# Performance work log

Hardware: AMD Instinct MI355X
Metric: run time of the kernel (lower is better)

The kernel has to match this reference:

```python
import jax, jax.numpy as jnp
import numpy as np

D_MODEL = 1024
NUM_HEADS = 16
HEAD_DIM = D_MODEL // NUM_HEADS
THETA = 10000.0


def apply_rope(x, token_positions):
    # x: [B, H, S, d_head]; token_positions: [S] int
    d = x.shape[-1]
    inv_freq = THETA ** (-jnp.arange(0, d, 2, dtype=jnp.float32) / d)  # [d/2]
    ang = token_positions.astype(jnp.float32)[:, None] * inv_freq      # [S, d/2]
    cos, sin = jnp.cos(ang), jnp.sin(ang)
    x1 = x[..., 0::2]
    x2 = x[..., 1::2]
    out_even = x1 * cos - x2 * sin
    out_odd = x1 * sin + x2 * cos
    # interleave even/odd back: [..., S, d/2, 2] -> [..., S, d]
    return jnp.stack([out_even, out_odd], axis=-1).reshape(x.shape)


def setup_inputs() -> dict:
    key = jax.random.key(0)
    ks = jax.random.split(key, 5)
    scale = 1.0 / np.sqrt(D_MODEL)
    x = jax.random.normal(ks[0], (4, 2048, D_MODEL), dtype=jnp.float32)
    wq = jax.random.normal(ks[1], (D_MODEL, D_MODEL), dtype=jnp.float32) * scale
    wk = jax.random.normal(ks[2], (D_MODEL, D_MODEL), dtype=jnp.float32) * scale
    wv = jax.random.normal(ks[3], (D_MODEL, D_MODEL), dtype=jnp.float32) * scale
    wo = jax.random.normal(ks[4], (D_MODEL, D_MODEL), dtype=jnp.float32) * scale
    token_positions = jnp.arange(2048, dtype=jnp.int32)
    return {"x": x, "wq": wq, "wk": wk, "wv": wv, "wo": wo,
            "token_positions": token_positions}


def reference(x, wq, wk, wv, wo, token_positions):
    B, S, D = x.shape
    H, dh = NUM_HEADS, HEAD_DIM
    # fused QKV projection (Linear stores weight [out, in]; y = x @ W.T)
    q = jnp.einsum('bsd,ed->bse', x, wq).reshape(B, S, H, dh).transpose(0, 2, 1, 3)
    k = jnp.einsum('bsd,ed->bse', x, wk).reshape(B, S, H, dh).transpose(0, 2, 1, 3)
    v = jnp.einsum('bsd,ed->bse', x, wv).reshape(B, S, H, dh).transpose(0, 2, 1, 3)
    q = apply_rope(q, token_positions)
    k = apply_rope(k, token_positions)
    scores = jnp.einsum('bhid,bhjd->bhij', q, k) / jnp.sqrt(jnp.float32(dh))
    causal = jnp.tril(jnp.ones((S, S), dtype=bool))
    scores = jnp.where(causal, scores, -jnp.inf)
    attn = jax.nn.softmax(scores, axis=-1)
    out = jnp.einsum('bhij,bhjd->bhid', attn, v)            # [B,H,S,dh]
    out = out.transpose(0, 2, 1, 3).reshape(B, S, D)         # [B,S,D]
    return jnp.einsum('bsd,ed->bse', out, wo)
```

## Files before the change

kernel.cpp:

```cpp
#include <hip/hip_runtime.h>
#include <cstdint>
#include <cstddef>

typedef short bf16x8 __attribute__((ext_vector_type(8)));
typedef float f32x4 __attribute__((ext_vector_type(4)));
typedef unsigned short u16;
typedef u16 u16x4v __attribute__((ext_vector_type(4)));

#define SEQ 2048

static __device__ __forceinline__ u16 f2bf(float f) {
  uint32_t u = __builtin_bit_cast(uint32_t, f);
  u += 0x7fffu + ((u >> 16) & 1u);
  return (u16)(u >> 16);
}
static __device__ __forceinline__ float bf2f(u16 v) {
  uint32_t u = ((uint32_t)v) << 16;
  return __builtin_bit_cast(float, u);
}

#define MFMA_BF16(a, b, c) __builtin_amdgcn_mfma_f32_16x16x32_bf16((a), (b), (c), 0, 0, 0)

static __device__ __forceinline__ void gload_lds16(const void* g, void* l) {
  __builtin_amdgcn_global_load_lds((const __attribute__((address_space(1))) void*)g,
                                   (__attribute__((address_space(3))) void*)l, 16, 0, 0);
}

__global__ __launch_bounds__(256) void cvt_kernel(
    const float4* __restrict__ x, const float4* __restrict__ wq,
    const float4* __restrict__ wk, const float4* __restrict__ wv,
    const float4* __restrict__ wo, u16x4v* __restrict__ xb,
    u16x4v* __restrict__ wqkvb, u16x4v* __restrict__ wob) {
  const int id = blockIdx.x * 256 + threadIdx.x;
  const float4* src;
  u16x4v* dst;
  if (id < 2097152) { src = x + id; dst = xb + id; }
  else if (id < 2359296) { const int j = id - 2097152; src = wq + j; dst = wqkvb + j; }
  else if (id < 2621440) { const int j = id - 2359296; src = wk + j; dst = wqkvb + 262144 + j; }
  else if (id < 2883584) { const int j = id - 2621440; src = wv + j; dst = wqkvb + 524288 + j; }
  else { const int j = id - 2883584; src = wo + j; dst = wob + j; }
  const float4 v = *src;
  u16x4v o;
  o[0] = f2bf(v.x); o[1] = f2bf(v.y); o[2] = f2bf(v.z); o[3] = f2bf(v.w);
  *dst = o;
}

__global__ __launch_bounds__(256) void rope_tbl_kernel(const int* __restrict__ tp,
                                                       float2* __restrict__ tbl) {
  const int id = blockIdx.x * 256 + threadIdx.x;
  const int s = id >> 5, i = id & 31;
  const float pos = (float)tp[s];
  const float freq = powf(10000.0f, -(float)(2 * i) / 64.0f);
  const float ang = pos * freq;
  float sv, cv;
  sincosf(ang, &sv, &cv);
  tbl[id] = make_float2(cv, sv);
}

template <bool OUT_BF16>
__global__ __launch_bounds__(256) void gemm_bt(const u16* __restrict__ A,
                                               const u16* __restrict__ Bt,
                                               void* __restrict__ Cout,
                                               int M, int N, int K) {
  __shared__ __align__(16) u16 As[128 * 64];
  __shared__ __align__(16) u16 Bs[128 * 64];
  const int tid = threadIdx.x;
  const int w = tid >> 6;
  const int l = tid & 63;
  const int g = l >> 4;
  const int lr = l & 15;
  const int wm = (w >> 1) * 64;
  const int wn = (w & 1) * 64;
  const long tile_m = (long)blockIdx.y * 128;
  const long tile_n = (long)blockIdx.x * 128;

  const int lrow = l >> 3;
  const int lcolsw = (l & 7) ^ lrow;

  f32x4 acc[4][4] = {};

  for (int k0 = 0; k0 < K; k0 += 64) {
#pragma unroll
    for (int cc = 0; cc < 4; ++cc) {
      const int c = w * 4 + cc;
      const int row = c * 8 + lrow;
      gload_lds16(A + (tile_m + row) * (long)K + k0 + lcolsw * 8, As + c * 512);
      gload_lds16(Bt + (tile_n + row) * (long)K + k0 + lcolsw * 8, Bs + c * 512);
    }
    __syncthreads();
#pragma unroll
    for (int kk = 0; kk < 2; ++kk) {
      bf16x8 af[4], bfr[4];
#pragma unroll
      for (int mi = 0; mi < 4; ++mi) {
        const int row = wm + mi * 16 + lr;
        const int cc = ((kk << 2) + g) ^ (row & 7);
        af[mi] = *(const bf16x8*)((const char*)As + row * 128 + cc * 16);
      }
#pragma unroll
      for (int ni = 0; ni < 4; ++ni) {
        const int row = wn + ni * 16 + lr;
        const int cc = ((kk << 2) + g) ^ (row & 7);
        bfr[ni] = *(const bf16x8*)((const char*)Bs + row * 128 + cc * 16);
      }
#pragma unroll
      for (int mi = 0; mi < 4; ++mi)
#pragma unroll
        for (int ni = 0; ni < 4; ++ni)
          acc[mi][ni] = MFMA_BF16(af[mi], bfr[ni], acc[mi][ni]);
    }
    __syncthreads();
  }

#pragma unroll
  for (int mi = 0; mi < 4; ++mi) {
#pragma unroll
    for (int ni = 0; ni < 4; ++ni) {
      const long row0 = tile_m + wm + mi * 16 + g * 4;
      const long col = tile_n + wn + ni * 16 + lr;
      if (OUT_BF16) {
        u16* C = (u16*)Cout;
#pragma unroll
        for (int r = 0; r < 4; ++r) C[(row0 + r) * N + col] = f2bf(acc[mi][ni][r]);
      } else {
        float* C = (float*)Cout;
#pragma unroll
        for (int r = 0; r < 4; ++r) C[(row0 + r) * N + col] = acc[mi][ni][r];
      }
    }
  }
}

__global__ __launch_bounds__(256) void rope_kernel(u16* __restrict__ qkvb,
                                                   const float2* __restrict__ tbl) {
  const int id = blockIdx.x * 256 + threadIdx.x;
  const int qk = id >> 22;
  const int r = id & 0x3FFFFF;
  const int row = r >> 9;
  const int p = r & 511;
  const int h = p >> 5, i = p & 31;
  const int s = row & (SEQ - 1);
  const float2 cs = tbl[s * 32 + i];
  uint32_t* ptr = (uint32_t*)(qkvb + (size_t)row * 3072 + qk * 1024 + h * 64 + 2 * i);
  const uint32_t v = *ptr;
  const float x1 = bf2f((u16)(v & 0xffffu));
  const float x2 = bf2f((u16)(v >> 16));
  const float e = x1 * cs.x - x2 * cs.y;
  const float o = x1 * cs.y + x2 * cs.x;
  *ptr = (uint32_t)f2bf(e) | ((uint32_t)f2bf(o) << 16);
}

__global__ __launch_bounds__(256) void transpose_v_kernel(const u16* __restrict__ qkvb,
                                                          u16* __restrict__ Vt) {
  const int bh = blockIdx.y;
  const int b = bh >> 4, h = bh & 15;
  const int s = blockIdx.x * 256 + threadIdx.x;
  const u16* src = qkvb + ((size_t)b * SEQ + s) * 3072 + 2048 + h * 64;
  u16* dst = Vt + (size_t)bh * 64 * SEQ + s;
#pragma unroll
  for (int d = 0; d < 64; ++d) dst[(size_t)d * SEQ] = src[d];
}

__global__ __launch_bounds__(256) void attn_kernel(const u16* __restrict__ qkvb,
                                                   const u16* __restrict__ Vt,
                                                   u16* __restrict__ attn_out) {
  const int tid = threadIdx.x;
  const int w = tid >> 6;
  const int l = tid & 63;
  const int g = l >> 4;
  const int lr = l & 15;
  const int bh = blockIdx.x;
  const int b = bh >> 4;
  const int h = bh & 15;
  const int qt = (int)gridDim.y - 1 - (int)blockIdx.y;
  const int wqb = qt * 128 + w * 32;

  const u16* Qb = qkvb + (size_t)b * SEQ * 3072 + h * 64;
  const u16* Kb = Qb + 1024;
  const u16* Vb = Vt + (size_t)bh * 64 * SEQ;

  const int krow0 = ((lr >> 2) << 3) + (lr & 3);

  bf16x8 qf[2][2];
#pragma unroll
  for (int s = 0; s < 2; ++s)
#pragma unroll
    for (int hf = 0; hf < 2; ++hf)
      qf[s][hf] = *(const bf16x8*)(Qb + (size_t)(wqb + s * 16 + lr) * 3072 + hf * 32 + g * 8);

  f32x4 O[2][4] = {};
  float m_s[2] = {-INFINITY, -INFINITY};
  float l_s[2] = {0.f, 0.f};

  const int nkt = (wqb >> 5) + 1;

  bf16x8 kf[2][2], vf[4];
#pragma unroll
  for (int kb = 0; kb < 2; ++kb)
#pragma unroll
    for (int hf = 0; hf < 2; ++hf)
      kf[kb][hf] = *(const bf16x8*)(Kb + (size_t)(krow0 + kb * 4) * 3072 + hf * 32 + g * 8);
#pragma unroll
  for (int dt = 0; dt < 4; ++dt)
    vf[dt] = *(const bf16x8*)(Vb + (size_t)(dt * 16 + lr) * SEQ + g * 8);

  for (int kt = 0; kt < nkt; ++kt) {
    const int kbase = kt * 32;
    bf16x8 kn[2][2], vn[4];
    {
      const int nb = kbase + 32;
#pragma unroll
      for (int kb = 0; kb < 2; ++kb)
#pragma unroll
        for (int hf = 0; hf < 2; ++hf)
          kn[kb][hf] = *(const bf16x8*)(Kb + (size_t)(nb + krow0 + kb * 4) * 3072 + hf * 32 + g * 8);
#pragma unroll
      for (int dt = 0; dt < 4; ++dt)
        vn[dt] = *(const bf16x8*)(Vb + (size_t)(dt * 16 + lr) * SEQ + nb + g * 8);
    }

    const bool diag = (kt == nkt - 1);
#pragma unroll
    for (int s = 0; s < 2; ++s) {
      f32x4 c0 = {0.f, 0.f, 0.f, 0.f}, c1 = {0.f, 0.f, 0.f, 0.f};
      c0 = MFMA_BF16(kf[0][0], qf[s][0], c0);
      c0 = MFMA_BF16(kf[0][1], qf[s][1], c0);
      c1 = MFMA_BF16(kf[1][0], qf[s][0], c1);
      c1 = MFMA_BF16(kf[1][1], qf[s][1], c1);
      const int q = wqb + s * 16 + lr;
      float pv[8];
#pragma unroll
      for (int r = 0; r < 4; ++r) {
        float v0 = c0[r] * 0.125f;
        float v1 = c1[r] * 0.125f;
        if (diag) {
          if (kbase + g * 8 + r > q) v0 = -1e30f;
          if (kbase + g * 8 + 4 + r > q) v1 = -1e30f;
        }
        pv[r] = v0;
        pv[4 + r] = v1;
      }
      float pm = pv[0];
#pragma unroll
      for (int i = 1; i < 8; ++i) pm = fmaxf(pm, pv[i]);
      pm = fmaxf(pm, __shfl_xor(pm, 16));
      pm = fmaxf(pm, __shfl_xor(pm, 32));
      const float mnew = fmaxf(m_s[s], pm);
      const float corr = __expf(m_s[s] - mnew);
      float psum = 0.f;
#pragma unroll
      for (int i = 0; i < 8; ++i) { pv[i] = __expf(pv[i] - mnew); psum += pv[i]; }
      psum += __shfl_xor(psum, 16);
      psum += __shfl_xor(psum, 32);
      l_s[s] = l_s[s] * corr + psum;
      m_s[s] = mnew;
#pragma unroll
      for (int dt = 0; dt < 4; ++dt)
#pragma unroll
        for (int r = 0; r < 4; ++r) O[s][dt][r] *= corr;

      bf16x8 pf;
#pragma unroll
      for (int j = 0; j < 8; ++j) pf[j] = (short)f2bf(pv[j]);
#pragma unroll
      for (int dt = 0; dt < 4; ++dt) O[s][dt] = MFMA_BF16(vf[dt], pf, O[s][dt]);
    }

#pragma unroll
    for (int kb = 0; kb < 2; ++kb)
#pragma unroll
      for (int hf = 0; hf < 2; ++hf) kf[kb][hf] = kn[kb][hf];
#pragma unroll
    for (int dt = 0; dt < 4; ++dt) vf[dt] = vn[dt];
  }

#pragma unroll
  for (int s = 0; s < 2; ++s) {
    const float inv = 1.0f / l_s[s];
    const int q = wqb + s * 16 + lr;
    u16* orow = attn_out + ((size_t)b * SEQ + q) * 1024 + h * 64;
#pragma unroll
    for (int dt = 0; dt < 4; ++dt) {
      u16x4v pk;
#pragma unroll
      for (int r = 0; r < 4; ++r) pk[r] = f2bf(O[s][dt][r] * inv);
      *(u16x4v*)(orow + dt * 16 + g * 4) = pk;
    }
  }
}

extern "C" void kernel_launch(void* const* d_in, const int* in_sizes, int n_in,
                              void* d_out, int out_size, void* d_ws, size_t ws_size,
                              hipStream_t stream) {
  const float* x = (const float*)d_in[0];
  const float* wq = (const float*)d_in[1];
  const float* wk = (const float*)d_in[2];
  const float* wv = (const float*)d_in[3];
  const float* wo = (const float*)d_in[4];
  const int* tp = (const int*)d_in[5];

  char* ws = (char*)d_ws;
  u16* xb       = (u16*)(ws + 0);
  u16* wqkvb    = (u16*)(ws + 16777216);
  u16* wob      = (u16*)(ws + 23068672);
  u16* qkvb     = (u16*)(ws + 25165824);
  u16* Vt       = (u16*)(ws + 75497472);
  u16* attn_out = (u16*)(ws + 92274688);
  float2* tbl   = (float2*)(ws + 109051904);

  cvt_kernel<<<12288, 256, 0, stream>>>((const float4*)x, (const float4*)wq,
                                        (const float4*)wk, (const float4*)wv,
                                        (const float4*)wo, (u16x4v*)xb,
                                        (u16x4v*)wqkvb, (u16x4v*)wob);
  rope_tbl_kernel<<<256, 256, 0, stream>>>(tp, tbl);
  gemm_bt<true><<<dim3(24, 64), 256, 0, stream>>>(xb, wqkvb, qkvb, 8192, 3072, 1024);
  rope_kernel<<<32768, 256, 0, stream>>>(qkvb, tbl);
  transpose_v_kernel<<<dim3(8, 64), 256, 0, stream>>>(qkvb, Vt);
  attn_kernel<<<dim3(64, 16), 256, 0, stream>>>(qkvb, Vt, attn_out);
  gemm_bt<false><<<dim3(8, 64), 256, 0, stream>>>(attn_out, wob, d_out, 8192, 1024, 1024);
}
```

Baseline: 348.4 us.

## Fuse RoPE and V transpose into QKV GEMM epilogue; restructure attention loop

Permutes the Q/K weight rows so each GEMM tile holds matching RoPE pairs, then applies RoPE and the softmax scale (with log2e folded in) in the QKV GEMM epilogue and writes V transposed directly. This removes the separate rope and transpose kernels and their extra memory passes. The attention kernel now processes 64-key tiles, uses exp2 with deferred max rescaling and packed bf16 conversion, and pairs two query tiles per block to balance the causal work. Costs are more register pressure and a skipped-rescale threshold that lets unnormalized values grow to a bounded range.

```diff
diff --git a/kernel.cpp b/kernel.cpp
--- a/kernel.cpp
+++ b/kernel.cpp
@@ -6,17 +6,22 @@
 typedef float f32x4 __attribute__((ext_vector_type(4)));
 typedef unsigned short u16;
 typedef u16 u16x4v __attribute__((ext_vector_type(4)));
+typedef uint32_t u32x4v __attribute__((ext_vector_type(4)));
 
 #define SEQ 2048
+#define QSCALE 0.18033688011112042f
+#define DEFER_THR 11.5415603f
 
 static __device__ __forceinline__ u16 f2bf(float f) {
   uint32_t u = __builtin_bit_cast(uint32_t, f);
   u += 0x7fffu + ((u >> 16) & 1u);
   return (u16)(u >> 16);
 }
-static __device__ __forceinline__ float bf2f(u16 v) {
-  uint32_t u = ((uint32_t)v) << 16;
-  return __builtin_bit_cast(float, u);
+
+static __device__ __forceinline__ uint32_t cvtpk_bf16(float lo, float hi) {
+  uint32_t r;
+  asm("v_cvt_pk_bf16_f32 %0, %1, %2" : "=v"(r) : "v"(lo), "v"(hi));
+  return r;
 }
 
 #define MFMA_BF16(a, b, c) __builtin_amdgcn_mfma_f32_16x16x32_bf16((a), (b), (c), 0, 0, 0)
@@ -35,9 +40,15 @@
   const float4* src;
   u16x4v* dst;
   if (id < 2097152) { src = x + id; dst = xb + id; }
-  else if (id < 2359296) { const int j = id - 2097152; src = wq + j; dst = wqkvb + j; }
-  else if (id < 2621440) { const int j = id - 2359296; src = wk + j; dst = wqkvb + 262144 + j; }
-  else if (id < 2883584) { const int j = id - 2621440; src = wv + j; dst = wqkvb + 524288 + j; }
+  else if (id < 2359296) {
+    const int j = id - 2097152; const int e = j >> 8;
+    const int ep = (e & ~63) | ((e & 63) >> 1) | ((e & 1) << 5);
+    src = wq + j; dst = wqkvb + ep * 256 + (j & 255);
+  } else if (id < 2621440) {
+    const int j = id - 2359296; const int e = j >> 8;
+    const int ep = (e & ~63) | ((e & 63) >> 1) | ((e & 1) << 5);
+    src = wk + j; dst = wqkvb + 262144 + ep * 256 + (j & 255);
+  } else if (id < 2883584) { const int j = id - 2621440; src = wv + j; dst = wqkvb + 524288 + j; }
   else { const int j = id - 2883584; src = wo + j; dst = wob + j; }
   const float4 v = *src;
   u16x4v o;
@@ -57,10 +68,12 @@
   tbl[id] = make_float2(cv, sv);
 }
 
-template <bool OUT_BF16>
+template <int MODE>
 __global__ __launch_bounds__(256) void gemm_bt(const u16* __restrict__ A,
                                                const u16* __restrict__ Bt,
                                                void* __restrict__ Cout,
+                                               u16* __restrict__ Vt,
+                                               const float2* __restrict__ tbl,
                                                int M, int N, int K) {
   __shared__ __align__(16) u16 As[128 * 64];
   __shared__ __align__(16) u16 Bs[128 * 64];
@@ -112,58 +125,62 @@
     __syncthreads();
   }
 
-#pragma unroll
-  for (int mi = 0; mi < 4; ++mi) {
-#pragma unroll
-    for (int ni = 0; ni < 4; ++ni) {
-      const long row0 = tile_m + wm + mi * 16 + g * 4;
-      const long col = tile_n + wn + ni * 16 + lr;
-      if (OUT_BF16) {
-        u16* C = (u16*)Cout;
-#pragma unroll
-        for (int r = 0; r < 4; ++r) C[(row0 + r) * N + col] = f2bf(acc[mi][ni][r]);
-      } else {
-        float* C = (float*)Cout;
+  if constexpr (MODE == 0) {
+    float* C = (float*)Cout;
+#pragma unroll
+    for (int mi = 0; mi < 4; ++mi) {
+#pragma unroll
+      for (int ni = 0; ni < 4; ++ni) {
+        const long row0 = tile_m + wm + mi * 16 + g * 4;
+        const long col = tile_n + wn + ni * 16 + lr;
 #pragma unroll
         for (int r = 0; r < 4; ++r) C[(row0 + r) * N + col] = acc[mi][ni][r];
       }
     }
+  } else {
+    u16* C = (u16*)Cout;
+    if (tile_n < 2048) {
+      const float scale = (tile_n < 1024) ? QSCALE : 1.0f;
+#pragma unroll
+      for (int mi = 0; mi < 4; ++mi) {
+        const long row0 = tile_m + wm + mi * 16 + g * 4;
+#pragma unroll
+        for (int np = 0; np < 2; ++np) {
+          const long col = tile_n + wn + np * 16 + lr;
+          const int i = (int)col & 31;
+#pragma unroll
+          for (int r = 0; r < 4; ++r) {
+            const long row = row0 + r;
+            const float2 cs = tbl[((int)row & (SEQ - 1)) * 32 + i];
+            const float x1 = acc[mi][np][r];
+            const float x2 = acc[mi][np + 2][r];
+            C[row * N + col]      = f2bf((x1 * cs.x - x2 * cs.y) * scale);
+            C[row * N + col + 32] = f2bf((x1 * cs.y + x2 * cs.x) * scale);
+          }
+        }
+      }
+    } else {
+#pragma unroll
+      for (int mi = 0; mi < 4; ++mi) {
+        const long row0 = tile_m + wm + mi * 16 + g * 4;
+        const int bb = (int)(row0 >> 11);
+        const int s0 = (int)row0 & (SEQ - 1);
+#pragma unroll
+        for (int ni = 0; ni < 4; ++ni) {
+          const int hd = (int)(tile_n + wn + ni * 16 + lr) - 2048;
+          u16x4v pk;
+#pragma unroll
+          for (int r = 0; r < 4; ++r) pk[r] = f2bf(acc[mi][ni][r]);
+          *(u16x4v*)(Vt + ((size_t)(bb * 16 + (hd >> 6)) * 64 + (hd & 63)) * SEQ + s0) = pk;
+        }
+      }
+    }
   }
 }
 
-__global__ __launch_bounds__(256) void rope_kernel(u16* __restrict__ qkvb,
-                                                   const float2* __restrict__ tbl) {
-  const int id = blockIdx.x * 256 + threadIdx.x;
-  const int qk = id >> 22;
-  const int r = id & 0x3FFFFF;
-  const int row = r >> 9;
-  const int p = r & 511;
-  const int h = p >> 5, i = p & 31;
-  const int s = row & (SEQ - 1);
-  const float2 cs = tbl[s * 32 + i];
-  uint32_t* ptr = (uint32_t*)(qkvb + (size_t)row * 3072 + qk * 1024 + h * 64 + 2 * i);
-  const uint32_t v = *ptr;
-  const float x1 = bf2f((u16)(v & 0xffffu));
-  const float x2 = bf2f((u16)(v >> 16));
-  const float e = x1 * cs.x - x2 * cs.y;
-  const float o = x1 * cs.y + x2 * cs.x;
-  *ptr = (uint32_t)f2bf(e) | ((uint32_t)f2bf(o) << 16);
-}
-
-__global__ __launch_bounds__(256) void transpose_v_kernel(const u16* __restrict__ qkvb,
-                                                          u16* __restrict__ Vt) {
-  const int bh = blockIdx.y;
-  const int b = bh >> 4, h = bh & 15;
-  const int s = blockIdx.x * 256 + threadIdx.x;
-  const u16* src = qkvb + ((size_t)b * SEQ + s) * 3072 + 2048 + h * 64;
-  u16* dst = Vt + (size_t)bh * 64 * SEQ + s;
-#pragma unroll
-  for (int d = 0; d < 64; ++d) dst[(size_t)d * SEQ] = src[d];
-}
-
-__global__ __launch_bounds__(256) void attn_kernel(const u16* __restrict__ qkvb,
-                                                   const u16* __restrict__ Vt,
-                                                   u16* __restrict__ attn_out) {
+__global__ __launch_bounds__(256, 2) void attn_kernel(const u16* __restrict__ qkvb,
+                                                      const u16* __restrict__ Vt,
+                                                      u16* __restrict__ attn_out) {
   const int tid = threadIdx.x;
   const int w = tid >> 6;
   const int l = tid & 63;
@@ -172,8 +189,6 @@
   const int bh = blockIdx.x;
   const int b = bh >> 4;
   const int h = bh & 15;
-  const int qt = (int)gridDim.y - 1 - (int)blockIdx.y;
-  const int wqb = qt * 128 + w * 32;
 
   const u16* Qb = qkvb + (size_t)b * SEQ * 3072 + h * 64;
   const u16* Kb = Qb + 1024;
@@ -181,110 +196,133 @@
 
   const int krow0 = ((lr >> 2) << 3) + (lr & 3);
 
-  bf16x8 qf[2][2];
-#pragma unroll
-  for (int s = 0; s < 2; ++s)
-#pragma unroll
-    for (int hf = 0; hf < 2; ++hf)
-      qf[s][hf] = *(const bf16x8*)(Qb + (size_t)(wqb + s * 16 + lr) * 3072 + hf * 32 + g * 8);
-
-  f32x4 O[2][4] = {};
-  float m_s[2] = {-INFINITY, -INFINITY};
-  float l_s[2] = {0.f, 0.f};
-
-  const int nkt = (wqb >> 5) + 1;
-
-  bf16x8 kf[2][2], vf[4];
-#pragma unroll
-  for (int kb = 0; kb < 2; ++kb)
-#pragma unroll
-    for (int hf = 0; hf < 2; ++hf)
-      kf[kb][hf] = *(const bf16x8*)(Kb + (size_t)(krow0 + kb * 4) * 3072 + hf * 32 + g * 8);
-#pragma unroll
-  for (int dt = 0; dt < 4; ++dt)
-    vf[dt] = *(const bf16x8*)(Vb + (size_t)(dt * 16 + lr) * SEQ + g * 8);
-
-  for (int kt = 0; kt < nkt; ++kt) {
-    const int kbase = kt * 32;
-    bf16x8 kn[2][2], vn[4];
-    {
-      const int nb = kbase + 32;
-#pragma unroll
-      for (int kb = 0; kb < 2; ++kb)
-#pragma unroll
-        for (int hf = 0; hf < 2; ++hf)
-          kn[kb][hf] = *(const bf16x8*)(Kb + (size_t)(nb + krow0 + kb * 4) * 3072 + hf * 32 + g * 8);
+#pragma unroll
+  for (int ph = 0; ph < 2; ++ph) {
+    const int qt = ph ? (int)blockIdx.y : 15 - (int)blockIdx.y;
+    const int wqb = qt * 128 + w * 32;
+
+    bf16x8 qf[2][2];
+#pragma unroll
+    for (int s = 0; s < 2; ++s)
+#pragma unroll
+      for (int hf = 0; hf < 2; ++hf)
+        qf[s][hf] = *(const bf16x8*)(Qb + (size_t)(wqb + s * 16 + lr) * 3072 + hf * 32 + g * 8);
+
+    f32x4 O[2][4] = {};
+    float m_s[2] = {-1e38f, -1e38f};
+    float l_s[2] = {0.f, 0.f};
+
+    const int n32 = (wqb >> 5) + 1;
+    const int n64 = (n32 + 1) >> 1;
+
+    bf16x8 kf[4][2];
+#pragma unroll
+    for (int X = 0; X < 4; ++X)
+#pragma unroll
+      for (int hf = 0; hf < 2; ++hf)
+        kf[X][hf] = *(const bf16x8*)(Kb + (size_t)((X >> 1) * 32 + krow0 + (X & 1) * 4) * 3072 + hf * 32 + g * 8);
+
+    for (int kt = 0; kt < n64; ++kt) {
+      const int kbase = kt * 64;
+      bf16x8 kn[4][2];
+      {
+        const int nb = kbase + 64;
+#pragma unroll
+        for (int X = 0; X < 4; ++X)
+#pragma unroll
+          for (int hf = 0; hf < 2; ++hf)
+            kn[X][hf] = *(const bf16x8*)(Kb + (size_t)(nb + (X >> 1) * 32 + krow0 + (X & 1) * 4) * 3072 + hf * 32 + g * 8);
+      }
+      bf16x8 vf[4][2];
 #pragma unroll
       for (int dt = 0; dt < 4; ++dt)
-        vn[dt] = *(const bf16x8*)(Vb + (size_t)(dt * 16 + lr) * SEQ + nb + g * 8);
-    }
-
-    const bool diag = (kt == nkt - 1);
+#pragma unroll
+        for (int hv = 0; hv < 2; ++hv)
+          vf[dt][hv] = *(const bf16x8*)(Vb + (size_t)(dt * 16 + lr) * SEQ + kbase + hv * 32 + g * 8);
+
+      const bool diag = (kt == n64 - 1);
+#pragma unroll
+      for (int s = 0; s < 2; ++s) {
+        f32x4 c[4] = {};
+#pragma unroll
+        for (int X = 0; X < 4; ++X) {
+          c[X] = MFMA_BF16(kf[X][0], qf[s][0], c[X]);
+          c[X] = MFMA_BF16(kf[X][1], qf[s][1], c[X]);
+        }
+        const int q = wqb + s * 16 + lr;
+        float t[16];
+#pragma unroll
+        for (int X = 0; X < 4; ++X)
+#pragma unroll
+          for (int r = 0; r < 4; ++r) {
+            float v = c[X][r];
+            if (diag) {
+              const int kk = kbase + (X >> 1) * 32 + g * 8 + (X & 1) * 4 + r;
+              if (kk > q) v = -1e30f;
+            }
+            t[X * 4 + r] = v;
+          }
+        float m01 = fmaxf(t[0], t[1]), m23 = fmaxf(t[2], t[3]);
+        float m45 = fmaxf(t[4], t[5]), m67 = fmaxf(t[6], t[7]);
+        float m89 = fmaxf(t[8], t[9]), mab = fmaxf(t[10], t[11]);
+        float mcd = fmaxf(t[12], t[13]), mef = fmaxf(t[14], t[15]);
+        float pm = fmaxf(fmaxf(fmaxf(m01, m23), fmaxf(m45, m67)),
+                         fmaxf(fmaxf(m89, mab), fmaxf(mcd, mef)));
+        pm = fmaxf(pm, __shfl_xor(pm, 16));
+        pm = fmaxf(pm, __shfl_xor(pm, 32));
+        if (!__all(pm <= m_s[s] + DEFER_THR)) {
+          const float mnew = fmaxf(m_s[s], pm);
+          const float corr = __builtin_amdgcn_exp2f(m_s[s] - mnew);
+          l_s[s] *= corr;
+#pragma unroll
+          for (int dt = 0; dt < 4; ++dt)
+#pragma unroll
+            for (int r = 0; r < 4; ++r) O[s][dt][r] *= corr;
+          m_s[s] = mnew;
+        }
+        float p[16];
+        float psum = 0.f;
+#pragma unroll
+        for (int i = 0; i < 16; ++i) {
+          p[i] = __builtin_amdgcn_exp2f(t[i] - m_s[s]);
+          psum += p[i];
+        }
+        psum += __shfl_xor(psum, 16);
+        psum += __shfl_xor(psum, 32);
+        l_s[s] += psum;
+
+        u32x4v pk0, pk1;
+#pragma unroll
+        for (int j = 0; j < 4; ++j) {
+          pk0[j] = cvtpk_bf16(p[2 * j], p[2 * j + 1]);
+          pk1[j] = cvtpk_bf16(p[8 + 2 * j], p[8 + 2 * j + 1]);
+        }
+        const bf16x8 pf0 = __builtin_bit_cast(bf16x8, pk0);
+        const bf16x8 pf1 = __builtin_bit_cast(bf16x8, pk1);
+#pragma unroll
+        for (int dt = 0; dt < 4; ++dt) {
+          O[s][dt] = MFMA_BF16(vf[dt][0], pf0, O[s][dt]);
+          O[s][dt] = MFMA_BF16(vf[dt][1], pf1, O[s][dt]);
+        }
+      }
+#pragma unroll
+      for (int X = 0; X < 4; ++X)
+#pragma unroll
+        for (int hf = 0; hf < 2; ++hf) kf[X][hf] = kn[X][hf];
+    }
+
 #pragma unroll
     for (int s = 0; s < 2; ++s) {
-      f32x4 c0 = {0.f, 0.f, 0.f, 0.f}, c1 = {0.f, 0.f, 0.f, 0.f};
-      c0 = MFMA_BF16(kf[0][0], qf[s][0], c0);
-      c0 = MFMA_BF16(kf[0][1], qf[s][1], c0);
-      c1 = MFMA_BF16(kf[1][0], qf[s][0], c1);
-      c1 = MFMA_BF16(kf[1][1], qf[s][1], c1);
+      const float inv = 1.0f / l_s[s];
       const int q = wqb + s * 16 + lr;
-      float pv[8];
-#pragma unroll
-      for (int r = 0; r < 4; ++r) {
-        float v0 = c0[r] * 0.125f;
-        float v1 = c1[r] * 0.125f;
-        if (diag) {
-          if (kbase + g * 8 + r > q) v0 = -1e30f;
-          if (kbase + g * 8 + 4 + r > q) v1 = -1e30f;
-        }
-        pv[r] = v0;
-        pv[4 + r] = v1;
-      }
-      float pm = pv[0];
-#pragma unroll
-      for (int i = 1; i < 8; ++i) pm = fmaxf(pm, pv[i]);
-      pm = fmaxf(pm, __shfl_xor(pm, 16));
-      pm = fmaxf(pm, __shfl_xor(pm, 32));
-      const float mnew = fmaxf(m_s[s], pm);
-      const float corr = __expf(m_s[s] - mnew);
-      float psum = 0.f;
-#pragma unroll
-      for (int i = 0; i < 8; ++i) { pv[i] = __expf(pv[i] - mnew); psum += pv[i]; }
-      psum += __shfl_xor(psum, 16);
-      psum += __shfl_xor(psum, 32);
-      l_s[s] = l_s[s] * corr + psum;
-      m_s[s] = mnew;
-#pragma unroll
-      for (int dt = 0; dt < 4; ++dt)
-#pragma unroll
-        for (int r = 0; r < 4; ++r) O[s][dt][r] *= corr;
-
-      bf16x8 pf;
-#pragma unroll
-      for (int j = 0; j < 8; ++j) pf[j] = (short)f2bf(pv[j]);
-#pragma unroll
-      for (int dt = 0; dt < 4; ++dt) O[s][dt] = MFMA_BF16(vf[dt], pf, O[s][dt]);
-    }
-
-#pragma unroll
-    for (int kb = 0; kb < 2; ++kb)
-#pragma unroll
-      for (int hf = 0; hf < 2; ++hf) kf[kb][hf] = kn[kb][hf];
-#pragma unroll
-    for (int dt = 0; dt < 4; ++dt) vf[dt] = vn[dt];
-  }
-
-#pragma unroll
-  for (int s = 0; s < 2; ++s) {
-    const float inv = 1.0f / l_s[s];
-    const int q = wqb + s * 16 + lr;
-    u16* orow = attn_out + ((size_t)b * SEQ + q) * 1024 + h * 64;
-#pragma unroll
-    for (int dt = 0; dt < 4; ++dt) {
-      u16x4v pk;
-#pragma unroll
-      for (int r = 0; r < 4; ++r) pk[r] = f2bf(O[s][dt][r] * inv);
-      *(u16x4v*)(orow + dt * 16 + g * 4) = pk;
+      u16* orow = attn_out + ((size_t)b * SEQ + q) * 1024 + h * 64;
+#pragma unroll
+      for (int dt = 0; dt < 4; ++dt) {
+        u16x4v pk;
+#pragma unroll
+        for (int r = 0; r < 4; ++r) pk[r] = f2bf(O[s][dt][r] * inv);
+        *(u16x4v*)(orow + dt * 16 + g * 4) = pk;
+      }
     }
   }
 }
@@ -313,9 +351,7 @@
                                         (const float4*)wo, (u16x4v*)xb,
                                         (u16x4v*)wqkvb, (u16x4v*)wob);
   rope_tbl_kernel<<<256, 256, 0, stream>>>(tp, tbl);
-  gemm_bt<true><<<dim3(24, 64), 256, 0, stream>>>(xb, wqkvb, qkvb, 8192, 3072, 1024);
-  rope_kernel<<<32768, 256, 0, stream>>>(qkvb, tbl);
-  transpose_v_kernel<<<dim3(8, 64), 256, 0, stream>>>(qkvb, Vt);
-  attn_kernel<<<dim3(64, 16), 256, 0, stream>>>(qkvb, Vt, attn_out);
-  gemm_bt<false><<<dim3(8, 64), 256, 0, stream>>>(attn_out, wob, d_out, 8192, 1024, 1024);
-}
+  gemm_bt<1><<<dim3(24, 64), 256, 0, stream>>>(xb, wqkvb, qkvb, Vt, tbl, 8192, 3072, 1024);
+  attn_kernel<<<dim3(64, 8), 256, 0, stream>>>(qkvb, Vt, attn_out);
+  gemm_bt<0><<<dim3(8, 64), 256, 0, stream>>>(attn_out, wob, d_out, nullptr, nullptr, 8192, 1024, 1024);
+}
```

After: 318.8 us. 1.09x faster.
